# Performance work log

Measured on AMD Instinct MI355X. Metric: run time of the kernel, lower is better.

Reference implementation:

```python
import jax, jax.numpy as jnp
import numpy as np

N_NODES = 50000
N_EDGES = 800000
NUM_GRAPHS = 256
D_COUNT = 9
BN_EPS = 1e-5
LRELU_SLOPE = 0.01


def _rbf(d):
    # d: [E]; linspace mu over [0, 6] with 9 centers, sigma = 6/9
    mu = jnp.linspace(0.0, 6.0, D_COUNT)  # [9]
    sigma = 6.0 / D_COUNT
    return jnp.exp(-(((d[:, None] - mu[None, :]) / sigma) ** 2))  # [E, 9]


def _interaction_layer(x, pos, row, col, Wc, bc, Wn, bn, g, be):
    # per-edge gather of positions, RBF radial embedding
    coord_diff = pos[row] - pos[col]                       # [E, 3]
    d = jnp.linalg.norm(coord_diff, axis=-1)               # [E]
    radial = jax.nn.silu(_rbf(d) @ Wc + bc)                # [E, C]
    # message = x_j * radial; scatter-add to target nodes (col)
    msg = x[row] * radial                                  # [E, C]
    agg = jax.ops.segment_sum(msg, col, num_segments=x.shape[0])  # [N, C]
    # mlp_node_cov: Linear -> Dropout(eval: identity) -> LeakyReLU -> BatchNorm1d(eval, fresh stats)
    h = (x + agg) @ Wn + bn
    h = jnp.where(h > 0, h, LRELU_SLOPE * h)
    h = g * h / jnp.sqrt(jnp.asarray(1.0 + BN_EPS, h.dtype)) + be
    return h


def setup_inputs() -> dict:
    key = jax.random.key(0)
    ks = jax.random.split(key, 16)
    C_IN, C_H = 64, 128
    inp = {
        "x": jax.random.normal(ks[0], (N_NODES, C_IN), jnp.float32),
        "pos": jax.random.normal(ks[1], (N_NODES, 3), jnp.float32) * 3.0,
        "edge_index": jax.random.randint(ks[2], (2, N_EDGES), 0, N_NODES, jnp.int32),
        "batch": jnp.sort(jax.random.randint(ks[3], (N_NODES,), 0, NUM_GRAPHS, jnp.int32)),
        "W_lin": jax.random.normal(ks[4], (C_IN, C_H), jnp.float32) / np.sqrt(C_IN),
        "b_lin": jnp.zeros((C_H,), jnp.float32),
    }
    for i, l in enumerate(("1", "2", "3")):
        kk = jax.random.split(ks[5 + i], 2)
        inp["Wc" + l] = jax.random.normal(kk[0], (D_COUNT, C_H), jnp.float32) / np.sqrt(D_COUNT)
        inp["bc" + l] = jnp.zeros((C_H,), jnp.float32)
        inp["Wn" + l] = jax.random.normal(kk[1], (C_H, C_H), jnp.float32) / np.sqrt(C_H)
        inp["bn" + l] = jnp.zeros((C_H,), jnp.float32)
        inp["g" + l] = jnp.ones((C_H,), jnp.float32)
        inp["be" + l] = jnp.zeros((C_H,), jnp.float32)
    return inp


def reference(x, pos, edge_index, batch, W_lin, b_lin,
              Wc1, bc1, Wn1, bn1, g1, be1,
              Wc2, bc2, Wn2, bn2, g2, be2,
              Wc3, bc3, Wn3, bn3, g3, be3):
    row, col = edge_index[0], edge_index[1]
    h = jax.nn.silu(x @ W_lin + b_lin)
    h = _interaction_layer(h, pos, row, col, Wc1, bc1, Wn1, bn1, g1, be1)
    h = _interaction_layer(h, pos, row, col, Wc2, bc2, Wn2, bn2, g2, be2)
    h = _interaction_layer(h, pos, row, col, Wc3, bc3, Wn3, bn3, g3, be3)
    # global_add_pool
    return jax.ops.segment_sum(h, batch, num_segments=NUM_GRAPHS)
```

## Files before the change

### kernel.cpp

```cpp
#include <hip/hip_runtime.h>
#include <hip/hip_fp16.h>
#include <math.h>

#define N_NODES 50000
#define N_EDGES 800000
#define NUM_GRAPHS 256
#define C_IN 64
#define C_H 128
#define D_COUNT 9
#define LRELU_SLOPE 0.01f
#define TAB_BINS 8192
#define TAB_SCALE 1024.0f
#define WEDGES 64
#define NCHUNK (N_EDGES / WEDGES)
#define NAGG (NCHUNK / 4)
#define NBUCK ((N_NODES + 255) / 256)
#define REGION_CAP 6144
#define SCAT_BLK_EDGES 2048
#define TBLK (TAB_BINS * 64 / 256)
#define WNBLK 8
#define ZBLK 1024
#define LIN0BLK ((N_NODES + 31) / 32)
#define OUTZBLK 32
#define OFF1 (3 * TBLK)
#define OFF2 (OFF1 + 3 * WNBLK)
#define OFF3 (OFF2 + ZBLK)
#define OFF4 (OFF3 + LIN0BLK)
#define OFF5 (OFF4 + OUTZBLK)
#define SETUP_GRID (OFF5 + 1)

typedef _Float16 half8_t __attribute__((ext_vector_type(8)));
typedef float f32x4_t __attribute__((ext_vector_type(4)));

__device__ __forceinline__ float fast_rcp(float x) { return __builtin_amdgcn_rcpf(x); }
__device__ __forceinline__ __half2 u2h2(unsigned int u) { return __builtin_bit_cast(__half2, u); }
__device__ __forceinline__ unsigned int h22u(__half2 h) { return __builtin_bit_cast(unsigned int, h); }

__device__ __forceinline__ void atomic_pk_add_h2(unsigned int* addr, unsigned int val) {
    asm volatile("global_atomic_pk_add_f16 %0, %1, off"
                 :: "v"(addr), "v"(val) : "memory");
}

__global__ __launch_bounds__(256) void setup_kernel(
        const float* __restrict__ Wc1, const float* __restrict__ bc1,
        const float* __restrict__ Wc2, const float* __restrict__ bc2,
        const float* __restrict__ Wc3, const float* __restrict__ bc3,
        const float* __restrict__ Wn1, const float* __restrict__ Wn2,
        const float* __restrict__ Wn3,
        const float* __restrict__ x, const float* __restrict__ Wl,
        const float* __restrict__ bl,
        unsigned int* __restrict__ tabh, unsigned int* __restrict__ Wnh,
        uint4* __restrict__ aggz, unsigned int* __restrict__ hhf,
        uint4* __restrict__ outz, int* __restrict__ bcur) {
    __shared__ float xs[32][C_IN];
    const int b = blockIdx.x;
    const int t = threadIdx.x;
    if (b < OFF1) {
        const int l = b / TBLK;
        const float* Wc = (l == 0) ? Wc1 : (l == 1) ? Wc2 : Wc3;
        const float* bc = (l == 0) ? bc1 : (l == 1) ? bc2 : bc3;
        const int idx = (b - l * TBLK) * 256 + t;
        const int lane = idx & 63;
        const int bin = idx >> 6;
        const float d = ((float)bin + 0.5f) * (1.0f / TAB_SCALE);
        float v[2];
#pragma unroll
        for (int p = 0; p < 2; ++p) {
            const int c = 2 * lane + p;
            float a = bc[c];
#pragma unroll
            for (int k = 0; k < D_COUNT; ++k) {
                const float u = (d - 0.75f * (float)k) * 1.5f;
                a = fmaf(__expf(-u * u), Wc[k * C_H + c], a);
            }
            v[p] = a * fast_rcp(1.0f + __expf(-a));
        }
        tabh[(size_t)l * TAB_BINS * 64 + idx] = h22u(__floats2half2_rn(v[0], v[1]));
    } else if (b < OFF2) {
        const int bb = b - OFF1;
        const int l = bb / WNBLK;
        const float* Wn = (l == 0) ? Wn1 : (l == 1) ? Wn2 : Wn3;
        const int idx = (bb - l * WNBLK) * 256 + t;
        const int lane = idx & 63;
        const int tile = idx >> 6;
        const int kc = tile >> 3, ct = tile & 7;
        const int q = lane >> 4, r = lane & 15;
        half8_t v;
#pragma unroll
        for (int j = 0; j < 8; ++j)
            v[j] = (_Float16)Wn[(size_t)(kc * 32 + 8 * q + j) * C_H + ct * 16 + r];
        ((uint4*)Wnh)[(size_t)l * 2048 + idx] = __builtin_bit_cast(uint4, v);
    } else if (b < OFF3) {
        const int n16 = N_NODES * 16;
        const int stride = ZBLK * 256;
        for (int i = (b - OFF2) * 256 + t; i < n16; i += stride)
            aggz[i] = make_uint4(0u, 0u, 0u, 0u);
    } else if (b < OFF4) {
        const int node0 = (b - OFF3) * 32;
        for (int i = t * 4; i < 32 * C_IN; i += 256 * 4) {
            const int n = i >> 6;
            const int c = i & 63;
            if (node0 + n < N_NODES)
                *(float4*)&xs[n][c] = *(const float4*)&x[(size_t)(node0 + n) * C_IN + c];
        }
        __syncthreads();
        const int wv = t >> 6;
        const int lane = t & 63;
        const int nb = wv * 8;
        const float2 b2 = *(const float2*)&bl[2 * lane];
        float2 acc[8];
#pragma unroll
        for (int n = 0; n < 8; ++n) acc[n] = b2;
        for (int k = 0; k < C_IN; k += 4) {
            const float2 w0 = *(const float2*)&Wl[(size_t)(k + 0) * C_H + 2 * lane];
            const float2 w1 = *(const float2*)&Wl[(size_t)(k + 1) * C_H + 2 * lane];
            const float2 w2 = *(const float2*)&Wl[(size_t)(k + 2) * C_H + 2 * lane];
            const float2 w3 = *(const float2*)&Wl[(size_t)(k + 3) * C_H + 2 * lane];
#pragma unroll
            for (int n = 0; n < 8; ++n) {
                const float4 sv = *(const float4*)&xs[nb + n][k];
                acc[n].x = fmaf(sv.x, w0.x, acc[n].x); acc[n].y = fmaf(sv.x, w0.y, acc[n].y);
                acc[n].x = fmaf(sv.y, w1.x, acc[n].x); acc[n].y = fmaf(sv.y, w1.y, acc[n].y);
                acc[n].x = fmaf(sv.z, w2.x, acc[n].x); acc[n].y = fmaf(sv.z, w2.y, acc[n].y);
                acc[n].x = fmaf(sv.w, w3.x, acc[n].x); acc[n].y = fmaf(sv.w, w3.y, acc[n].y);
            }
        }
#pragma unroll
        for (int n = 0; n < 8; ++n) {
            const int node = node0 + nb + n;
            if (node < N_NODES) {
                const float ax = acc[n].x, ay = acc[n].y;
                const float sx = ax * fast_rcp(1.0f + __expf(-ax));
                const float sy = ay * fast_rcp(1.0f + __expf(-ay));
                hhf[(size_t)node * 64 + lane] = h22u(__floats2half2_rn(sx, sy));
            }
        }
    } else if (b < OFF5) {
        const int n16 = NUM_GRAPHS * C_H / 4;
        const int stride = OUTZBLK * 256;
        for (int i = (b - OFF4) * 256 + t; i < n16; i += stride)
            outz[i] = make_uint4(0u, 0u, 0u, 0u);
    } else {
        if (t < NBUCK) bcur[t] = 0;
    }
}

__global__ __launch_bounds__(256) void bscatter_kernel(
        const int* __restrict__ row, const int* __restrict__ col,
        const float* __restrict__ pos, int* __restrict__ bcur, uint2* __restrict__ ebuf) {
    __shared__ int lhist[NBUCK];
    __shared__ int lcur[NBUCK];
    const int t = threadIdx.x;
    const int e0 = blockIdx.x * SCAT_BLK_EDGES;
    for (int i = t; i < NBUCK; i += 256) lhist[i] = 0;
    __syncthreads();

    int myb[8];
    uint2 myrec[8];
#pragma unroll
    for (int s = 0; s < 8; ++s) {
        const int e = e0 + s * 256 + t;
        if (e < N_EDGES) {
            const int r = row[e];
            const int c = col[e];
            const float dx = pos[r * 3 + 0] - pos[c * 3 + 0];
            const float dy = pos[r * 3 + 1] - pos[c * 3 + 1];
            const float dz = pos[r * 3 + 2] - pos[c * 3 + 2];
            const float d = sqrtf(dx * dx + dy * dy + dz * dz);
            int bin = (int)(d * TAB_SCALE);
            bin = bin < TAB_BINS - 1 ? bin : TAB_BINS - 1;
            myb[s] = c >> 8;
            myrec[s] = make_uint2((unsigned int)r | ((unsigned int)c << 16),
                                  (unsigned int)bin);
            atomicAdd(&lhist[myb[s]], 1);
        } else {
            myb[s] = -1;
        }
    }
    __syncthreads();
    for (int i = t; i < NBUCK; i += 256)
        lcur[i] = (lhist[i] > 0) ? atomicAdd(&bcur[i], lhist[i]) : 0;
    __syncthreads();
#pragma unroll
    for (int s = 0; s < 8; ++s) {
        if (myb[s] >= 0) {
            const int p = atomicAdd(&lcur[myb[s]], 1);
            ebuf[(size_t)myb[s] * REGION_CAP + p] = myrec[s];
        }
    }
}

__global__ __launch_bounds__(256) void bsort_kernel(
        const uint2* __restrict__ ebuf, const int* __restrict__ bcur,
        uint2* __restrict__ rcb) {
    __shared__ uint2 se[REGION_CAP];
    __shared__ int lhist[256];
    __shared__ int lcur[256];
    __shared__ int csc[256];
    const int b = blockIdx.x;
    const int t = threadIdx.x;
    csc[t] = (t < NBUCK) ? bcur[t] : 0;
    __syncthreads();
    for (int d = 1; d < 256; d <<= 1) {
        const int x = (t >= d) ? csc[t - d] : 0;
        __syncthreads();
        csc[t] += x;
        __syncthreads();
    }
    const int dbase = (b == 0) ? 0 : csc[b - 1];
    const int n = bcur[b];

    const uint2* src = ebuf + (size_t)b * REGION_CAP;
    for (int i = t; i < n; i += 256) se[i] = src[i];
    lhist[t] = 0;
    __syncthreads();
    for (int i = t; i < n; i += 256)
        atomicAdd(&lhist[(se[i].x >> 16) & 255u], 1);
    __syncthreads();
    int v = lhist[t];
    int sv = v;
    lcur[t] = v;
    __syncthreads();
    for (int d = 1; d < 256; d <<= 1) {
        const int x = (t >= d) ? lcur[t - d] : 0;
        __syncthreads();
        lcur[t] += x;
        __syncthreads();
        sv = lcur[t];
    }
    __syncthreads();
    lcur[t] = sv - v;
    __syncthreads();
    for (int i = t; i < n; i += 256) {
        const uint2 e = se[i];
        const int dst = atomicAdd(&lcur[(e.x >> 16) & 255u], 1);
        rcb[dbase + dst] = e;
    }
}

__global__ __launch_bounds__(256) void aggregate_kernel(
        const unsigned int* __restrict__ hhf, const uint2* __restrict__ rcb,
        const unsigned int* __restrict__ tabh, unsigned int* __restrict__ aggh) {
    const int bid = blockIdx.x;
    const int xcd = bid & 7, ix = bid >> 3;
    const int qq = NAGG >> 3, rr = NAGG & 7;
    const int blk = (xcd < rr ? xcd * (qq + 1) : rr * (qq + 1) + (xcd - rr) * qq) + ix;
    const int t = threadIdx.x;
    const int lane = t & 63;
    const int wv = __builtin_amdgcn_readfirstlane(t >> 6);
    const size_t base = (size_t)(blk * 4 + wv) * WEDGES;

    const __half2 hzero = __floats2half2_rn(0.0f, 0.0f);

    unsigned int huA[8], huB[8], huC[8], huD[8];
    unsigned int tvA[8], tvB[8], tvC[8], tvD[8];
    int colA[8], colB[8], colC[8], colD[8];
    __half2 acc2 = hzero;
    float2 accf = make_float2(0.0f, 0.0f);
    int sCur;
    bool first = true;

#define LOADG(g, HU, TV, CO)                                                  \
    {                                                                         \
        _Pragma("unroll")                                                     \
        for (int u = 0; u < 8; ++u) {                                         \
            const uint2 m = rcb[base + (g) * 8 + u];                          \
            const unsigned int rcu = __builtin_amdgcn_readfirstlane(m.x);     \
            const int sBin = __builtin_amdgcn_readfirstlane((int)m.y);        \
            const int sRow = (int)(rcu & 0xffffu);                            \
            CO[u] = (int)(rcu >> 16);                                         \
            HU[u] = hhf[(size_t)sRow * 64 + lane];                            \
            TV[u] = tabh[(size_t)sBin * 64 + lane];                           \
        }                                                                     \
    }

#define COMPUTEG(HU, TV, CO)                                                  \
    {                                                                         \
        _Pragma("unroll")                                                     \
        for (int u = 0; u < 8; ++u) {                                         \
            if (CO[u] != sCur) {                                              \
                const float2 pf = __half22float2(acc2);                       \
                accf.x += pf.x; accf.y += pf.y; acc2 = hzero;                 \
                unsigned int* dst = &aggh[(size_t)sCur * 64 + lane];          \
                const unsigned int hv = h22u(__floats2half2_rn(accf.x, accf.y)); \
                if (first) {                                                  \
                    atomic_pk_add_h2(dst, hv);                                \
                    first = false;                                            \
                } else {                                                      \
                    *dst = hv;                                                \
                }                                                             \
                accf.x = 0.0f; accf.y = 0.0f;                                 \
                sCur = CO[u];                                                 \
            }                                                                 \
            acc2 = __hfma2(u2h2(HU[u]), u2h2(TV[u]), acc2);                   \
        }                                                                     \
        const float2 pg = __half22float2(acc2);                               \
        accf.x += pg.x; accf.y += pg.y; acc2 = hzero;                         \
    }

    LOADG(0, huA, tvA, colA);
    LOADG(1, huB, tvB, colB);
    LOADG(2, huC, tvC, colC);
    LOADG(3, huD, tvD, colD);
    sCur = colA[0];
    COMPUTEG(huA, tvA, colA);
    LOADG(4, huA, tvA, colA);
    COMPUTEG(huB, tvB, colB);
    LOADG(5, huB, tvB, colB);
    COMPUTEG(huC, tvC, colC);
    LOADG(6, huC, tvC, colC);
    COMPUTEG(huD, tvD, colD);
    LOADG(7, huD, tvD, colD);
    COMPUTEG(huA, tvA, colA);
    COMPUTEG(huB, tvB, colB);
    COMPUTEG(huC, tvC, colC);
    COMPUTEG(huD, tvD, colD);

    {
        unsigned int* dst = &aggh[(size_t)sCur * 64 + lane];
        atomic_pk_add_h2(dst, h22u(__floats2half2_rn(accf.x, accf.y)));
    }
#undef LOADG
#undef COMPUTEG
}

template <int POOL, int ZERO>
__global__ __launch_bounds__(256) void node_kernel(
        unsigned int* __restrict__ hhf, unsigned int* __restrict__ aggh,
        const uint4* __restrict__ Wnb, const float* __restrict__ bn,
        const float* __restrict__ g, const float* __restrict__ be,
        const int* __restrict__ batch, float* __restrict__ out) {
    __shared__ unsigned short sA[32 * 136];
    const int node0 = blockIdx.x * 32;
    const int t = threadIdx.x;
    const uint4* hh4 = (const uint4*)hhf;
    uint4* ag4 = (uint4*)aggh;
    for (int i = t; i < 32 * 16; i += 256) {
        const int n = i >> 4;
        const int pp = i & 15;
        const int node = node0 + n;
        uint4 hv, av;
        if (node < N_NODES) {
            hv = hh4[(size_t)node * 16 + pp];
            av = ag4[(size_t)node * 16 + pp];
            if (ZERO) ag4[(size_t)node * 16 + pp] = make_uint4(0u, 0u, 0u, 0u);
        } else {
            hv = make_uint4(0u, 0u, 0u, 0u);
            av = hv;
        }
        uint4 sv;
        sv.x = h22u(__hadd2(u2h2(hv.x), u2h2(av.x)));
        sv.y = h22u(__hadd2(u2h2(hv.y), u2h2(av.y)));
        sv.z = h22u(__hadd2(u2h2(hv.z), u2h2(av.z)));
        sv.w = h22u(__hadd2(u2h2(hv.w), u2h2(av.w)));
        *(uint4*)&sA[n * 136 + 8 * pp] = sv;
    }
    __syncthreads();
    const int lane = t & 63;
    const int wv = t >> 6;
    const int q = lane >> 4;
    const int r = lane & 15;
    const int ct0 = 2 * wv, ct1 = 2 * wv + 1;
    const int c0 = ct0 * 16 + r, c1 = ct1 * 16 + r;
    const float bn0 = bn[c0], bn1 = bn[c1];
    f32x4_t acc00 = {bn0, bn0, bn0, bn0};
    f32x4_t acc01 = {bn1, bn1, bn1, bn1};
    f32x4_t acc10 = {bn0, bn0, bn0, bn0};
    f32x4_t acc11 = {bn1, bn1, bn1, bn1};
#pragma unroll
    for (int kc = 0; kc < 4; ++kc) {
        const half8_t a0 = __builtin_bit_cast(half8_t,
            *(const uint4*)&sA[(size_t)r * 136 + kc * 32 + 8 * q]);
        const half8_t a1 = __builtin_bit_cast(half8_t,
            *(const uint4*)&sA[(size_t)(16 + r) * 136 + kc * 32 + 8 * q]);
        const half8_t b0 = __builtin_bit_cast(half8_t, Wnb[(kc * 8 + ct0) * 64 + lane]);
        const half8_t b1 = __builtin_bit_cast(half8_t, Wnb[(kc * 8 + ct1) * 64 + lane]);
        acc00 = __builtin_amdgcn_mfma_f32_16x16x32_f16(a0, b0, acc00, 0, 0, 0);
        acc01 = __builtin_amdgcn_mfma_f32_16x16x32_f16(a0, b1, acc01, 0, 0, 0);
        acc10 = __builtin_amdgcn_mfma_f32_16x16x32_f16(a1, b0, acc10, 0, 0, 0);
        acc11 = __builtin_amdgcn_mfma_f32_16x16x32_f16(a1, b1, acc11, 0, 0, 0);
    }
    const float inv = 0.9999950000374997f;
    const float gv0 = g[c0] * inv, gv1 = g[c1] * inv;
    const float be0 = be[c0], be1 = be[c1];
    if (POOL == 0) {
        unsigned short* hp = (unsigned short*)hhf;
#pragma unroll
        for (int rt = 0; rt < 2; ++rt) {
            const f32x4_t aA = rt ? acc10 : acc00;
            const f32x4_t aB = rt ? acc11 : acc01;
#pragma unroll
            for (int i = 0; i < 4; ++i) {
                const int node = node0 + rt * 16 + 4 * q + i;
                if (node < N_NODES) {
                    float v0 = aA[i]; v0 = v0 > 0.0f ? v0 : LRELU_SLOPE * v0;
                    float v1 = aB[i]; v1 = v1 > 0.0f ? v1 : LRELU_SLOPE * v1;
                    hp[(size_t)node * C_H + c0] =
                        __builtin_bit_cast(unsigned short, (_Float16)fmaf(gv0, v0, be0));
                    hp[(size_t)node * C_H + c1] =
                        __builtin_bit_cast(unsigned short, (_Float16)fmaf(gv1, v1, be1));
                }
            }
        }
    } else {
        float pacc0 = 0.0f, pacc1 = 0.0f;
        int curb = -1;
#pragma unroll
        for (int rt = 0; rt < 2; ++rt) {
            const f32x4_t aA = rt ? acc10 : acc00;
            const f32x4_t aB = rt ? acc11 : acc01;
#pragma unroll
            for (int i = 0; i < 4; ++i) {
                const int node = node0 + rt * 16 + 4 * q + i;
                if (node < N_NODES) {
                    float v0 = aA[i]; v0 = v0 > 0.0f ? v0 : LRELU_SLOPE * v0;
                    float v1 = aB[i]; v1 = v1 > 0.0f ? v1 : LRELU_SLOPE * v1;
                    const float o0 = fmaf(gv0, v0, be0);
                    const float o1 = fmaf(gv1, v1, be1);
                    const int bb = batch[node];
                    if (bb != curb) {
                        if (curb >= 0) {
                            atomicAdd(&out[curb * C_H + c0], pacc0);
                            atomicAdd(&out[curb * C_H + c1], pacc1);
                        }
                        pacc0 = 0.0f; pacc1 = 0.0f;
                        curb = bb;
                    }
                    pacc0 += o0;
                    pacc1 += o1;
                }
            }
        }
        if (curb >= 0) {
            atomicAdd(&out[curb * C_H + c0], pacc0);
            atomicAdd(&out[curb * C_H + c1], pacc1);
        }
    }
}

extern "C" void kernel_launch(void* const* d_in, const int* in_sizes, int n_in,
                              void* d_out, int out_size, void* d_ws, size_t ws_size,
                              hipStream_t stream) {
    const float* x     = (const float*)d_in[0];
    const float* pos   = (const float*)d_in[1];
    const int*   eidx  = (const int*)d_in[2];
    const int*   batch = (const int*)d_in[3];
    const float* W_lin = (const float*)d_in[4];
    const float* b_lin = (const float*)d_in[5];

    unsigned int* aggh = (unsigned int*)d_ws;
    unsigned int* hhf  = aggh + (size_t)N_NODES * 64;
    unsigned int* Wnh  = hhf + (size_t)N_NODES * 64;
    unsigned int* tabh = Wnh + 3 * C_H * 64;
    int* bcur = (int*)(tabh + 3 * (size_t)TAB_BINS * 64);
    uintptr_t p = (uintptr_t)(bcur + NBUCK);
    p = (p + 15) & ~(uintptr_t)15;
    uint2* ebuf = (uint2*)p;
    uint2* rcb  = ebuf + (size_t)NBUCK * REGION_CAP;

    const int* row = eidx;
    const int* col = eidx + N_EDGES;

    hipLaunchKernelGGL(setup_kernel, dim3(SETUP_GRID), dim3(256), 0, stream,
                       (const float*)d_in[6],  (const float*)d_in[7],
                       (const float*)d_in[12], (const float*)d_in[13],
                       (const float*)d_in[18], (const float*)d_in[19],
                       (const float*)d_in[8],  (const float*)d_in[14],
                       (const float*)d_in[20],
                       x, W_lin, b_lin,
                       tabh, Wnh, (uint4*)aggh, hhf, (uint4*)d_out, bcur);

    hipLaunchKernelGGL(bscatter_kernel,
                       dim3((N_EDGES + SCAT_BLK_EDGES - 1) / SCAT_BLK_EDGES), dim3(256),
                       0, stream, row, col, pos, bcur, ebuf);
    hipLaunchKernelGGL(bsort_kernel, dim3(NBUCK), dim3(256), 0, stream,
                       ebuf, bcur, rcb);

    for (int l = 0; l < 3; ++l) {
        const float* bn = (const float*)d_in[6 + l * 6 + 3];
        const float* g  = (const float*)d_in[6 + l * 6 + 4];
        const float* be = (const float*)d_in[6 + l * 6 + 5];
        unsigned int* tab_l = tabh + (size_t)l * TAB_BINS * 64;
        const uint4* Wnb_l = (const uint4*)Wnh + (size_t)l * 2048;

        hipLaunchKernelGGL(aggregate_kernel, dim3(NAGG), dim3(256), 0, stream,
                           hhf, rcb, tab_l, aggh);
        if (l < 2) {
            hipLaunchKernelGGL(HIP_KERNEL_NAME(node_kernel<0, 1>),
                               dim3((N_NODES + 31) / 32), dim3(256), 0, stream,
                               hhf, aggh, Wnb_l, bn, g, be, batch, (float*)d_out);
        } else {
            hipLaunchKernelGGL(HIP_KERNEL_NAME(node_kernel<1, 0>),
                               dim3((N_NODES + 31) / 32), dim3(256), 0, stream,
                               hhf, aggh, Wnb_l, bn, g, be, batch, (float*)d_out);
        }
    }
}
```

Measured before the change: 211.2 us.

## Process two edges per wavefront with half-wave 8-byte gathers in aggregate

Restructures the edge aggregation kernel so each wavefront handles two edges per step: lanes 0-31 gather one edge's feature and table row and lanes 32-63 gather the other, each lane loading 8 bytes instead of 4. Segment flushes combine the two halves with cross-lane shuffles before a single half of lanes writes or atomically adds the packed half2 results. Edge metadata is read as 16-byte pairs, and the pipeline drops from four to three register buffers. The aim is fewer, wider memory instructions and fewer loop iterations, at the cost of extra shuffles and divergent branching when the two edges target different nodes.

```diff
diff --git a/kernel.cpp b/kernel.cpp
--- a/kernel.cpp
+++ b/kernel.cpp
@@ -248,80 +248,123 @@
     const int t = threadIdx.x;
     const int lane = t & 63;
     const int wv = __builtin_amdgcn_readfirstlane(t >> 6);
-    const size_t base = (size_t)(blk * 4 + wv) * WEDGES;
-
+    const size_t ebase = (size_t)(blk * 4 + wv) * WEDGES;
+    const int lidx = lane & 31;
+    const bool lo = lane < 32;
+
+    const uint2* hh2 = (const uint2*)hhf;
+    const uint2* tb2 = (const uint2*)tabh;
     const __half2 hzero = __floats2half2_rn(0.0f, 0.0f);
 
-    unsigned int huA[8], huB[8], huC[8], huD[8];
-    unsigned int tvA[8], tvB[8], tvC[8], tvD[8];
-    int colA[8], colB[8], colC[8], colD[8];
-    __half2 acc2 = hzero;
-    float2 accf = make_float2(0.0f, 0.0f);
+    uint2 huA[4], huB[4], huC[4];
+    uint2 tvA[4], tvB[4], tvC[4];
+    int c0A[4], c1A[4], c0B[4], c1B[4], c0C[4], c1C[4];
+    __half2 acc2a = hzero, acc2b = hzero;
+    float2 accfA = make_float2(0.0f, 0.0f);
+    float2 accfB = make_float2(0.0f, 0.0f);
     int sCur;
     bool first = true;
 
-#define LOADG(g, HU, TV, CO)                                                  \
+#define FLUSHSEG()                                                            \
+    {                                                                         \
+        {                                                                     \
+            const float2 pa = __half22float2(acc2a);                          \
+            const float2 pb = __half22float2(acc2b);                          \
+            accfA.x += pa.x; accfA.y += pa.y;                                 \
+            accfB.x += pb.x; accfB.y += pb.y;                                 \
+            acc2a = hzero; acc2b = hzero;                                     \
+        }                                                                     \
+        const float cax = accfA.x + __shfl_xor(accfA.x, 32);                  \
+        const float cay = accfA.y + __shfl_xor(accfA.y, 32);                  \
+        const float cbx = accfB.x + __shfl_xor(accfB.x, 32);                  \
+        const float cby = accfB.y + __shfl_xor(accfB.y, 32);                  \
+        if (lo) {                                                             \
+            unsigned int* dst = &aggh[(size_t)sCur * 64 + 2 * lidx];          \
+            const unsigned int va = h22u(__floats2half2_rn(cax, cay));        \
+            const unsigned int vb = h22u(__floats2half2_rn(cbx, cby));        \
+            if (first) {                                                      \
+                atomic_pk_add_h2(dst, va);                                    \
+                atomic_pk_add_h2(dst + 1, vb);                                \
+            } else {                                                          \
+                dst[0] = va;                                                  \
+                dst[1] = vb;                                                  \
+            }                                                                 \
+        }                                                                     \
+        first = false;                                                        \
+        accfA = make_float2(0.0f, 0.0f);                                      \
+        accfB = make_float2(0.0f, 0.0f);                                      \
+    }
+
+#define LOADG(g, HU, TV, C0, C1)                                              \
     {                                                                         \
         _Pragma("unroll")                                                     \
-        for (int u = 0; u < 8; ++u) {                                         \
-            const uint2 m = rcb[base + (g) * 8 + u];                          \
-            const unsigned int rcu = __builtin_amdgcn_readfirstlane(m.x);     \
-            const int sBin = __builtin_amdgcn_readfirstlane((int)m.y);        \
-            const int sRow = (int)(rcu & 0xffffu);                            \
-            CO[u] = (int)(rcu >> 16);                                         \
-            HU[u] = hhf[(size_t)sRow * 64 + lane];                            \
-            TV[u] = tabh[(size_t)sBin * 64 + lane];                           \
+        for (int u = 0; u < 4; ++u) {                                         \
+            const uint4 mm = *(const uint4*)&rcb[ebase + ((g) * 4 + u) * 2];  \
+            const unsigned int r0 = __builtin_amdgcn_readfirstlane(mm.x);     \
+            const int b0 = __builtin_amdgcn_readfirstlane((int)mm.y);         \
+            const unsigned int r1 = __builtin_amdgcn_readfirstlane(mm.z);     \
+            const int b1 = __builtin_amdgcn_readfirstlane((int)mm.w);         \
+            C0[u] = (int)(r0 >> 16);                                          \
+            C1[u] = (int)(r1 >> 16);                                          \
+            const int srow = lo ? (int)(r0 & 0xffffu) : (int)(r1 & 0xffffu);  \
+            const int sbin = lo ? b0 : b1;                                    \
+            HU[u] = hh2[(size_t)srow * 32 + lidx];                            \
+            TV[u] = tb2[(size_t)sbin * 32 + lidx];                            \
         }                                                                     \
     }
 
-#define COMPUTEG(HU, TV, CO)                                                  \
+#define COMPUTEG(HU, TV, C0, C1)                                              \
     {                                                                         \
         _Pragma("unroll")                                                     \
-        for (int u = 0; u < 8; ++u) {                                         \
-            if (CO[u] != sCur) {                                              \
-                const float2 pf = __half22float2(acc2);                       \
-                accf.x += pf.x; accf.y += pf.y; acc2 = hzero;                 \
-                unsigned int* dst = &aggh[(size_t)sCur * 64 + lane];          \
-                const unsigned int hv = h22u(__floats2half2_rn(accf.x, accf.y)); \
-                if (first) {                                                  \
-                    atomic_pk_add_h2(dst, hv);                                \
-                    first = false;                                            \
-                } else {                                                      \
-                    *dst = hv;                                                \
+        for (int u = 0; u < 4; ++u) {                                         \
+            const int c0 = C0[u], c1 = C1[u];                                 \
+            if (c0 != sCur) { FLUSHSEG(); sCur = c0; }                        \
+            const bool same = (c0 == c1);                                     \
+            if (same || lo) {                                                 \
+                acc2a = __hfma2(u2h2(HU[u].x), u2h2(TV[u].x), acc2a);         \
+                acc2b = __hfma2(u2h2(HU[u].y), u2h2(TV[u].y), acc2b);         \
+            }                                                                 \
+            if (!same) {                                                      \
+                FLUSHSEG();                                                   \
+                sCur = c1;                                                    \
+                if (!lo) {                                                    \
+                    acc2a = __hfma2(u2h2(HU[u].x), u2h2(TV[u].x), acc2a);     \
+                    acc2b = __hfma2(u2h2(HU[u].y), u2h2(TV[u].y), acc2b);     \
                 }                                                             \
-                accf.x = 0.0f; accf.y = 0.0f;                                 \
-                sCur = CO[u];                                                 \
             }                                                                 \
-            acc2 = __hfma2(u2h2(HU[u]), u2h2(TV[u]), acc2);                   \
         }                                                                     \
-        const float2 pg = __half22float2(acc2);                               \
-        accf.x += pg.x; accf.y += pg.y; acc2 = hzero;                         \
-    }
-
-    LOADG(0, huA, tvA, colA);
-    LOADG(1, huB, tvB, colB);
-    LOADG(2, huC, tvC, colC);
-    LOADG(3, huD, tvD, colD);
-    sCur = colA[0];
-    COMPUTEG(huA, tvA, colA);
-    LOADG(4, huA, tvA, colA);
-    COMPUTEG(huB, tvB, colB);
-    LOADG(5, huB, tvB, colB);
-    COMPUTEG(huC, tvC, colC);
-    LOADG(6, huC, tvC, colC);
-    COMPUTEG(huD, tvD, colD);
-    LOADG(7, huD, tvD, colD);
-    COMPUTEG(huA, tvA, colA);
-    COMPUTEG(huB, tvB, colB);
-    COMPUTEG(huC, tvC, colC);
-    COMPUTEG(huD, tvD, colD);
-
-    {
-        unsigned int* dst = &aggh[(size_t)sCur * 64 + lane];
-        atomic_pk_add_h2(dst, h22u(__floats2half2_rn(accf.x, accf.y)));
-    }
+        {                                                                     \
+            const float2 pa = __half22float2(acc2a);                          \
+            const float2 pb = __half22float2(acc2b);                          \
+            accfA.x += pa.x; accfA.y += pa.y;                                 \
+            accfB.x += pb.x; accfB.y += pb.y;                                 \
+            acc2a = hzero; acc2b = hzero;                                     \
+        }                                                                     \
+    }
+
+    LOADG(0, huA, tvA, c0A, c1A);
+    LOADG(1, huB, tvB, c0B, c1B);
+    LOADG(2, huC, tvC, c0C, c1C);
+    sCur = c0A[0];
+    COMPUTEG(huA, tvA, c0A, c1A);
+    LOADG(3, huA, tvA, c0A, c1A);
+    COMPUTEG(huB, tvB, c0B, c1B);
+    LOADG(4, huB, tvB, c0B, c1B);
+    COMPUTEG(huC, tvC, c0C, c1C);
+    LOADG(5, huC, tvC, c0C, c1C);
+    COMPUTEG(huA, tvA, c0A, c1A);
+    LOADG(6, huA, tvA, c0A, c1A);
+    COMPUTEG(huB, tvB, c0B, c1B);
+    LOADG(7, huB, tvB, c0B, c1B);
+    COMPUTEG(huC, tvC, c0C, c1C);
+    COMPUTEG(huA, tvA, c0A, c1A);
+    COMPUTEG(huB, tvB, c0B, c1B);
+
+    first = true;
+    FLUSHSEG();
 #undef LOADG
 #undef COMPUTEG
+#undef FLUSHSEG
 }
 
 template <int POOL, int ZERO>
```

Measured after the change: 221.3 us. 4.8% more time.
